# Kernel tuning notes

Measured on AMD Instinct MI355X. Metric: run time of the kernel, lower is better.

Reference implementation:

```python
import jax, jax.numpy as jnp
import numpy as np

BN_EPS = 1e-5

def conv2d(x, w, pad):
    return jax.lax.conv_general_dilated(x, w, (1, 1), [(pad, pad), (pad, pad)],
                                        dimension_numbers=('NCHW', 'OIHW', 'NCHW'))

def bn(x, g, b, m, v):
    # eval-mode batchnorm with running stats
    c = (None, slice(None), None, None)
    return g[c] * (x - m[c]) * jax.lax.rsqrt(v[c] + BN_EPS) + b[c]

def criss_cross_attention(x, wq, wk, wv, gamma):
    # x: (B, C, H, W); q/k have reduced dim d = C//8
    B, C, H, W = x.shape
    q = jnp.einsum('bchw,dc->bdhw', x, wq)
    k = jnp.einsum('bchw,dc->bdhw', x, wk)
    v = jnp.einsum('bchw,dc->bdhw', x, wv)
    # column (vertical) affinities: for each (h,w), keys at (k,w) -> (B,H,W,H)
    eH = jnp.einsum('bdhw,bdkw->bhwk', q, k)
    # -inf on the h==k diagonal (avoid counting the center pixel twice)
    eH = eH + jnp.where(jnp.eye(H, dtype=bool), -jnp.inf, 0.0)[None, :, None, :]
    # row (horizontal) affinities: keys at (h,k) -> (B,H,W,W)
    eW = jnp.einsum('bdhw,bdhk->bhwk', q, k)
    att = jax.nn.softmax(jnp.concatenate([eH, eW], axis=3), axis=3)  # (B,H,W,H+W)
    aH, aW = att[..., :H], att[..., H:]
    oH = jnp.einsum('bhwk,bdkw->bdhw', aH, v)
    oW = jnp.einsum('bhwk,bdhk->bdhw', aW, v)
    return gamma * (oH + oW) + x

def upsample_bilinear_align_corners(x, out_h, out_w):
    # torch nn.Upsample(mode='bilinear', align_corners=True)
    def interp(x, size, axis):
        n = x.shape[axis]
        pos = jnp.arange(size, dtype=x.dtype) * ((n - 1) / (size - 1))
        lo = jnp.floor(pos).astype(jnp.int32)
        hi = jnp.minimum(lo + 1, n - 1)
        w = pos - lo.astype(x.dtype)
        shp = [1] * x.ndim; shp[axis] = size
        w = w.reshape(shp)
        return jnp.take(x, lo, axis=axis) * (1 - w) + jnp.take(x, hi, axis=axis) * w
    x = interp(x, out_h, 2)
    return interp(x, out_w, 3)

def setup_inputs() -> dict:
    key = jax.random.key(0)
    ks = jax.random.split(key, 16)
    B, C, H, W = 2, 2048, 96, 96
    ic = C // 32          # inter_c = 64
    dq = ic // 8          # 8
    nc = 19
    s = 0.05
    return {
        'x': jax.random.normal(ks[0], (B, C, H, W), jnp.float32),
        'w_in': jax.random.normal(ks[1], (ic, C, 3, 3), jnp.float32) * s,
        'bn_in_g': jnp.ones((ic,), jnp.float32),
        'bn_in_b': jnp.zeros((ic,), jnp.float32),
        'bn_in_m': jax.random.normal(ks[2], (ic,), jnp.float32) * 0.1,
        'bn_in_v': jax.random.uniform(ks[3], (ic,), jnp.float32, 0.5, 1.5),
        'wq': jax.random.normal(ks[4], (dq, ic), jnp.float32) * s,
        'wk': jax.random.normal(ks[5], (dq, ic), jnp.float32) * s,
        'wv': jax.random.normal(ks[6], (ic, ic), jnp.float32) * s,
        'cca_gamma': jax.random.uniform(ks[7], (1,), jnp.float32, 0.2, 0.8),
        'w_out': jax.random.normal(ks[8], (ic, ic, 3, 3), jnp.float32) * s,
        'bn_out_g': jnp.ones((ic,), jnp.float32),
        'bn_out_b': jnp.zeros((ic,), jnp.float32),
        'bn_out_m': jax.random.normal(ks[9], (ic,), jnp.float32) * 0.1,
        'bn_out_v': jax.random.uniform(ks[10], (ic,), jnp.float32, 0.5, 1.5),
        'w_cls1': jax.random.normal(ks[11], (ic, C + ic, 3, 3), jnp.float32) * s,
        'bn_cls_g': jnp.ones((ic,), jnp.float32),
        'bn_cls_b': jnp.zeros((ic,), jnp.float32),
        'bn_cls_m': jax.random.normal(ks[12], (ic,), jnp.float32) * 0.1,
        'bn_cls_v': jax.random.uniform(ks[13], (ic,), jnp.float32, 0.5, 1.5),
        'w_cls2': jax.random.normal(ks[14], (nc, ic, 1, 1), jnp.float32) * s,
    }

def reference(x, w_in, bn_in_g, bn_in_b, bn_in_m, bn_in_v,
              wq, wk, wv, cca_gamma,
              w_out, bn_out_g, bn_out_b, bn_out_m, bn_out_v,
              w_cls1, bn_cls_g, bn_cls_b, bn_cls_m, bn_cls_v, w_cls2):
    RECURRENCE = 2
    out = jax.nn.relu(bn(conv2d(x, w_in, 1), bn_in_g, bn_in_b, bn_in_m, bn_in_v))
    for _ in range(RECURRENCE):
        out = criss_cross_attention(out, wq, wk, wv, cca_gamma)
    out = jax.nn.relu(bn(conv2d(out, w_out, 1), bn_out_g, bn_out_b, bn_out_m, bn_out_v))
    out = jnp.concatenate([x, out], axis=1)
    # cls_seg: conv -> BN (no relu) -> upsample x8 (bilinear, align_corners) -> 1x1 conv
    out = bn(conv2d(out, w_cls1, 1), bn_cls_g, bn_cls_b, bn_cls_m, bn_cls_v)
    H, W = out.shape[2], out.shape[3]
    out = upsample_bilinear_align_corners(out, H * 8, W * 8)
    out = conv2d(out, w_cls2, 0)
    return out
```

## Files before the change

### kernel.cpp

```cpp
#include <hip/hip_runtime.h>
#include <stdint.h>

#define HW 9216

typedef float f32x4 __attribute__((ext_vector_type(4)));
typedef short s16x8 __attribute__((ext_vector_type(8)));

#define PIN() asm volatile("" ::: "memory")
#define WAITV12() asm volatile("s_waitcnt vmcnt(12)" ::: "memory")

__device__ __forceinline__ unsigned short f2bf(float f){
  union { float fv; uint32_t u; } x; x.fv = f;
  uint32_t u = x.u;
  u += 0x7fffu + ((u >> 16) & 1u);
  return (unsigned short)(u >> 16);
}
__device__ __forceinline__ float bf2f(unsigned short s){
  union { uint32_t u; float fv; } x; x.u = ((uint32_t)s) << 16;
  return x.fv;
}

__device__ __forceinline__ void gload16(const void* g, void* l){
  __builtin_amdgcn_global_load_lds(
    (const __attribute__((address_space(1))) unsigned int*)g,
    (__attribute__((address_space(3))) unsigned int*)l, 16, 0, 0);
}

__global__ __launch_bounds__(256) void transp_kernel(const float* __restrict__ x,
    unsigned short* __restrict__ xT){
  __shared__ unsigned short tl[256 * 66];
  int blk = blockIdx.x;
  int b = blk / 1152; int r = blk - b * 1152;
  int cchunk = r / 144, pxt = r - cchunk * 144;
  int c0 = cchunk * 256, px0 = pxt * 64;
  int tid = threadIdx.x;
  for (int e = tid; e < 4096; e += 256){
    int cc = e >> 4, pq = e & 15;
    float4 v4 = *(const float4*)(x + ((size_t)(b * 2048 + c0 + cc)) * HW + px0 + pq * 4);
    const float* vp = (const float*)&v4;
    #pragma unroll
    for (int j = 0; j < 4; j++) tl[cc * 66 + pq * 4 + j] = f2bf(vp[j]);
  }
  __syncthreads();
  for (int j = tid; j < 2048; j += 256){
    int px = j >> 5, oct = j & 31;
    s16x8 pk;
    #pragma unroll
    for (int t = 0; t < 8; t++) pk[t] = (short)tl[(oct * 8 + t) * 66 + px];
    *(s16x8*)(xT + ((size_t)(b * 9216 + px0 + px)) * 2048 + c0 + oct * 8) = pk;
  }
}

__global__ void packw_kernel(const float* __restrict__ w, unsigned short* __restrict__ Wp, int Cin){
  int total = 64 * Cin * 9;
  for (int i = blockIdx.x * blockDim.x + threadIdx.x; i < total; i += gridDim.x * blockDim.x){
    int c = i & 31; int r = i >> 5; int o = r & 63; int r2 = r >> 6;
    int tap = r2 % 9; int ck = r2 / 9;
    Wp[i] = f2bf(w[((size_t)o * Cin + ck * 32 + c) * 9 + tap]);
  }
}

template<int T>
__device__ __forceinline__ void tapbody(const char* hb, s16x8 (&bs)[4], f32x4 (&acc)[4][4],
    const unsigned short* wbase, int gmax, int g0, int wv, int ln, int kg){
  constexpr int dy = T / 3, dx = T - dy * 3;
  #pragma unroll
  for (int mf = 0; mf < 4; mf++){
    int p = (wv * 4 + mf + dy) * 18 + (ln + dx);
    int aoff = p * 64 + ((kg ^ (p & 3)) << 4);
    s16x8 a = *(const s16x8*)(hb + aoff);
    #pragma unroll
    for (int nf = 0; nf < 4; nf++)
      acc[mf][nf] = __builtin_amdgcn_mfma_f32_16x16x32_bf16(a, bs[nf], acc[mf][nf], 0, 0, 0);
  }
  constexpr int dck = (T + 3) / 9, dt = (T + 3) % 9;
  if (g0 + T + 3 < gmax){
    const unsigned short* wb2 = wbase + dck * 18432 + dt * 2048;
    #pragma unroll
    for (int nf = 0; nf < 4; nf++) bs[nf] = *(const s16x8*)(wb2 + nf * 512);
  }
}

__global__ __launch_bounds__(256, 2) void conv_nhwc_kernel(
    const unsigned short* __restrict__ A0, int c0stride,
    const unsigned short* __restrict__ A1, int nck0,
    const unsigned short* __restrict__ Wp,
    unsigned short* __restrict__ sl, int nchunks,
    const unsigned short* __restrict__ zp){
  int mt = blockIdx.x;
  int b = mt / 36; int r = mt - b * 36;
  int h0 = (r / 6) * 16, w0 = (r % 6) * 16;
  int KS = gridDim.y, ks = blockIdx.y;
  int c0 = (nchunks * ks) / KS, c1 = (nchunks * (ks + 1)) / KS;
  int tid = threadIdx.x, lane = tid & 63, wv = tid >> 6;
  int ln = lane & 15, kg = lane >> 4;
  __shared__ char halo[2][24576];

  int pixb0[6], pixb1[6]; bool val[6];
  #pragma unroll
  for (int rr = 0; rr < 6; rr++){
    int i = tid + rr * 256;
    int p = i >> 2, q_lds = i & 3;
    int logq = q_lds ^ (p & 3);
    int hh = p / 18, ww = p - hh * 18;
    int h = h0 - 1 + hh, w = w0 - 1 + ww;
    bool v = (i < 1296) && ((unsigned)h < 96u) && ((unsigned)w < 96u);
    val[rr] = v;
    int pix = (b * 96 + h) * 96 + w;
    pixb0[rr] = v ? (pix * c0stride * 2 + logq * 16) : 0;
    pixb1[rr] = v ? (pix * 128 + logq * 16) : 0;
  }
  const char* a0B = (const char*)A0;
  const char* a1B = (const char*)A1;
  const char* zpB = (const char*)zp;

  auto stage = [&](char* ldsB, int ck){
    bool inA0 = (ck < nck0);
    int chb0 = ck * 64, chb1 = (ck - nck0) * 64;
    #pragma unroll
    for (int rr = 0; rr < 6; rr++){
      const char* src = zpB;
      if (val[rr]) src = inA0 ? (a0B + pixb0[rr] + chb0) : (a1B + pixb1[rr] + chb1);
      gload16(src, ldsB + (tid + rr * 256) * 16);
    }
  };

  f32x4 acc[4][4];
  #pragma unroll
  for (int i = 0; i < 4; i++)
    #pragma unroll
    for (int j = 0; j < 4; j++) acc[i][j] = (f32x4)(0.f);

  s16x8 bs0[4], bs1[4], bs2[4];
  int gmax = (c1 - c0) * 9;

  stage(&halo[0][0], c0);
  PIN();
  {
    const unsigned short* w0b = Wp + (size_t)c0 * 18432 + ln * 32 + kg * 8;
    #pragma unroll
    for (int nf = 0; nf < 4; nf++){
      bs0[nf] = *(const s16x8*)(w0b + 0 * 2048 + nf * 512);
      bs1[nf] = *(const s16x8*)(w0b + 1 * 2048 + nf * 512);
      bs2[nf] = *(const s16x8*)(w0b + 2 * 2048 + nf * 512);
    }
  }
  WAITV12();
  __builtin_amdgcn_s_barrier();

  for (int ck = c0; ck < c1; ck++){
    int cur = (ck - c0) & 1;
    if (ck + 1 < c1){ stage(&halo[cur ^ 1][0], ck + 1); PIN(); }
    const unsigned short* wbase = Wp + (size_t)ck * 18432 + ln * 32 + kg * 8;
    const char* hb = &halo[cur][0];
    int g0 = (ck - c0) * 9;
    tapbody<0>(hb, bs0, acc, wbase, gmax, g0, wv, ln, kg);
    tapbody<1>(hb, bs1, acc, wbase, gmax, g0, wv, ln, kg);
    tapbody<2>(hb, bs2, acc, wbase, gmax, g0, wv, ln, kg);
    tapbody<3>(hb, bs0, acc, wbase, gmax, g0, wv, ln, kg);
    tapbody<4>(hb, bs1, acc, wbase, gmax, g0, wv, ln, kg);
    tapbody<5>(hb, bs2, acc, wbase, gmax, g0, wv, ln, kg);
    tapbody<6>(hb, bs0, acc, wbase, gmax, g0, wv, ln, kg);
    tapbody<7>(hb, bs1, acc, wbase, gmax, g0, wv, ln, kg);
    tapbody<8>(hb, bs2, acc, wbase, gmax, g0, wv, ln, kg);
    if (ck + 1 < c1){
      WAITV12();
      __builtin_amdgcn_s_barrier();
    }
  }

  unsigned short* base = sl + ((size_t)(ks * 72 + mt)) * 16384;
  #pragma unroll
  for (int mf = 0; mf < 4; mf++)
    #pragma unroll
    for (int nf = 0; nf < 4; nf++){
      int o = nf * 16 + ln;
      #pragma unroll
      for (int rr = 0; rr < 4; rr++){
        int m = wv * 64 + mf * 16 + kg * 4 + rr;
        base[m * 64 + o] = f2bf(acc[mf][nf][rr]);
      }
    }
}

__global__ __launch_bounds__(256) void bn_reduce_kernel(const unsigned short* __restrict__ sl,
    int KS, const float* __restrict__ g, const float* __restrict__ bb,
    const float* __restrict__ mm, const float* __restrict__ vv, int relu,
    unsigned short* __restrict__ out){
  int idx = blockIdx.x * 256 + threadIdx.x;
  int mt = idx >> 14, e = idx & 16383;
  int m = e >> 6, o = e & 63;
  float s = 0.f;
  for (int ks = 0; ks < KS; ks++) s += bf2f(sl[((size_t)(ks * 72 + mt)) * 16384 + e]);
  float sc = g[o] * rsqrtf(vv[o] + 1e-5f);
  float valf = (s - mm[o]) * sc + bb[o];
  if (relu) valf = fmaxf(valf, 0.f);
  int b = mt / 36; int r = mt - b * 36;
  int h = (r / 6) * 16 + (m >> 4), w = (r % 6) * 16 + (m & 15);
  out[(((size_t)b * 96 + h) * 96 + w) * 64 + o] = f2bf(valf);
}

__global__ __launch_bounds__(256) void bn_reduce_cls_kernel(const unsigned short* __restrict__ sl,
    int KS, const float* __restrict__ g, const float* __restrict__ bb,
    const float* __restrict__ mm, const float* __restrict__ vv,
    const float* __restrict__ w2, float* __restrict__ t19){
  __shared__ float yl[4][64];
  __shared__ float w2L[19 * 64];
  int tid = threadIdx.x;
  for (int i = tid; i < 1216; i += 256) w2L[i] = w2[i];
  int idx = blockIdx.x * 256 + tid;
  int mt = idx >> 14, e = idx & 16383;
  int o = e & 63;
  float s = 0.f;
  for (int ks = 0; ks < KS; ks++) s += bf2f(sl[((size_t)(ks * 72 + mt)) * 16384 + e]);
  float sc = g[o] * rsqrtf(vv[o] + 1e-5f);
  float valf = (s - mm[o]) * sc + bb[o];
  yl[tid >> 6][o] = valf;
  __syncthreads();
  if (tid < 76){
    int mq = tid / 19, j = tid - mq * 19;
    float a = 0.f;
    #pragma unroll 8
    for (int c = 0; c < 64; c++) a += w2L[j * 64 + c] * yl[mq][c];
    int m = ((blockIdx.x & 63) << 2) + mq;
    int b = mt / 36; int r = mt - b * 36;
    int h = (r / 6) * 16 + (m >> 4), w = (r % 6) * 16 + (m & 15);
    t19[((size_t)(b * 19 + j)) * HW + h * 96 + w] = a;
  }
}

__global__ __launch_bounds__(128) void cca_proj_kernel(const unsigned short* __restrict__ xin,
    const float* __restrict__ wq, const float* __restrict__ wk, const float* __restrict__ wv,
    float* __restrict__ q, float* __restrict__ k, float* __restrict__ v){
  __shared__ float wqL[512], wkL[512], wvL[4096];
  int tid = threadIdx.x;
  for (int i = tid; i < 512; i += 128){ wqL[i] = wq[i]; wkL[i] = wk[i]; }
  for (int i = tid; i < 4096; i += 128) wvL[i] = wv[i];
  __syncthreads();
  int gp = blockIdx.x * 128 + tid;
  unsigned short xv16[64];
  #pragma unroll
  for (int t = 0; t < 8; t++)
    *(s16x8*)(&xv16[t * 8]) = *(const s16x8*)(xin + (size_t)gp * 64 + t * 8);
  float qa[8], ka[8], va[64];
  #pragma unroll
  for (int d = 0; d < 8; d++){ qa[d] = 0.f; ka[d] = 0.f; }
  #pragma unroll
  for (int d = 0; d < 64; d++) va[d] = 0.f;
  #pragma unroll 4
  for (int c = 0; c < 64; c++){
    float xv = bf2f(xv16[c]);
    #pragma unroll
    for (int d = 0; d < 8; d++){ qa[d] += wqL[d * 64 + c] * xv; ka[d] += wkL[d * 64 + c] * xv; }
    #pragma unroll
    for (int d = 0; d < 64; d++) va[d] += wvL[d * 64 + c] * xv;
  }
  #pragma unroll
  for (int d = 0; d < 8; d++){ q[(size_t)gp * 8 + d] = qa[d]; k[(size_t)gp * 8 + d] = ka[d]; }
  #pragma unroll
  for (int d = 0; d < 64; d++) v[(size_t)gp * 64 + d] = va[d];
}

__global__ __launch_bounds__(256, 2) void cca_colE_kernel(const float* __restrict__ qT,
    const float* __restrict__ kT, float* __restrict__ ebuf){
  int blk = blockIdx.x; int b = blk / 96, w = blk - b * 96;
  __shared__ float qcL[96 * 12], kcL[96 * 12];
  int tid = threadIdx.x;
  for (int i = tid; i < 768; i += 256){
    int hp = i >> 3, d = i & 7;
    size_t gidx = ((size_t)(b * HW) + hp * 96 + w) * 8 + d;
    qcL[hp * 12 + d] = qT[gidx];
    kcL[hp * 12 + d] = kT[gidx];
  }
  __syncthreads();
  int hb = tid & 15, kb2 = tid >> 4;
  int h0 = hb * 6, kp0 = kb2 * 6;
  f32x4 q0[6], q1[6], k0[6], k1[6];
  #pragma unroll
  for (int i = 0; i < 6; i++){
    q0[i] = *(const f32x4*)&qcL[(h0 + i) * 12];
    q1[i] = *(const f32x4*)&qcL[(h0 + i) * 12 + 4];
    k0[i] = *(const f32x4*)&kcL[(kp0 + i) * 12];
    k1[i] = *(const f32x4*)&kcL[(kp0 + i) * 12 + 4];
  }
  #pragma unroll
  for (int i = 0; i < 6; i++){
    size_t rbase = (((size_t)b * 96 + (h0 + i)) * 96 + w) * 96;
    #pragma unroll
    for (int j = 0; j < 6; j++){
      float e = 0.f;
      #pragma unroll
      for (int d = 0; d < 4; d++) e += q0[i][d] * k0[j][d] + q1[i][d] * k1[j][d];
      ebuf[rbase + kp0 + j] = (kp0 + j == h0 + i) ? -1e30f : e;
    }
  }
}

__global__ __launch_bounds__(256, 1) void cca_rowSM_kernel(const float* __restrict__ qT,
    const float* __restrict__ kT, const float* __restrict__ vT,
    const unsigned short* __restrict__ xin, const float* __restrict__ gamma,
    float* __restrict__ ebuf, unsigned short* __restrict__ xout){
  int blk = blockIdx.x; int b = blk / 96, h = blk - b * 96;
  __shared__ float qrL[96 * 12], krL[96 * 12];
  __shared__ float ewT[96 * 102];
  __shared__ unsigned short vL2[96 * 68];
  __shared__ unsigned short aW[96 * 100];
  int tid = threadIdx.x;
  int lane = tid & 63, wvid = tid >> 6;
  size_t rowb = (size_t)(b * HW) + h * 96;
  const float* ebase = ebuf + rowb * 96;

  float pre0[24], pre1[24];
  #pragma unroll
  for (int t = 0; t < 24; t++){
    int w = wvid + t * 4;
    pre0[t] = ebase[(size_t)w * 96 + lane];
    pre1[t] = (lane < 32) ? ebase[(size_t)w * 96 + 64 + lane] : 0.f;
  }

  for (int i = tid; i < 768; i += 256){
    int wp = i >> 3, d = i & 7;
    qrL[wp * 12 + d] = qT[(rowb + wp) * 8 + d];
    krL[wp * 12 + d] = kT[(rowb + wp) * 8 + d];
  }
  for (int i = tid; i < 6144; i += 256){
    int wp = i >> 6, d = i & 63;
    vL2[wp * 68 + d] = f2bf(vT[(rowb + wp) * 64 + d]);
  }
  __syncthreads();
  {
    int wb_ = tid & 15, kb_ = tid >> 4;
    int w0 = wb_ * 6, kp0 = kb_ * 6;
    f32x4 q0[6], q1[6], k0[6], k1[6];
    #pragma unroll
    for (int i = 0; i < 6; i++){
      q0[i] = *(const f32x4*)&qrL[(w0 + i) * 12];
      q1[i] = *(const f32x4*)&qrL[(w0 + i) * 12 + 4];
      k0[i] = *(const f32x4*)&krL[(kp0 + i) * 12];
      k1[i] = *(const f32x4*)&krL[(kp0 + i) * 12 + 4];
    }
    #pragma unroll
    for (int j = 0; j < 6; j++)
      #pragma unroll
      for (int i = 0; i < 6; i++){
        float e = 0.f;
        #pragma unroll
        for (int d = 0; d < 4; d++) e += q0[i][d] * k0[j][d] + q1[i][d] * k1[j][d];
        ewT[(kp0 + j) * 102 + (w0 + i)] = e;
      }
  }
  __syncthreads();
  #pragma unroll
  for (int t = 0; t < 24; t++){
    int w = wvid + t * 4;
    float x0 = pre0[t];
    float x1 = (lane < 32) ? pre1[t] : ewT[(lane - 32) * 102 + w];
    float x2 = ewT[(lane + 32) * 102 + w];
    float mx = fmaxf(x0, fmaxf(x1, x2));
    #pragma unroll
    for (int s = 32; s; s >>= 1) mx = fmaxf(mx, __shfl_xor(mx, s));
    float e0 = __expf(x0 - mx), e1 = __expf(x1 - mx), e2 = __expf(x2 - mx);
    float sm = e0 + e1 + e2;
    #pragma unroll
    for (int s = 32; s; s >>= 1) sm += __shfl_xor(sm, s);
    float inv = 1.f / sm;
    float* ebw = (float*)(ebase + (size_t)w * 96);
    ebw[lane] = e0 * inv;
    if (lane < 32) ebw[64 + lane] = e1 * inv;
    else           aW[(lane - 32) * 100 + w] = f2bf(e1 * inv);
    aW[(lane + 32) * 100 + w] = f2bf(e2 * inv);
  }
  __syncthreads();
  float gm = gamma[0];
  int d0 = (tid & 15) * 4, w0 = (tid >> 4) * 6;
  f32x4 acc2[6];
  #pragma unroll
  for (int c = 0; c < 6; c++) acc2[c] = (f32x4)(0.f);
  for (int kp = 0; kp < 96; kp++){
    ushort4 vv4 = *(const ushort4*)&vL2[kp * 68 + d0];
    f32x4 vf; vf[0] = bf2f(vv4.x); vf[1] = bf2f(vv4.y); vf[2] = bf2f(vv4.z); vf[3] = bf2f(vv4.w);
    ushort2 a01 = *(const ushort2*)&aW[kp * 100 + w0];
    ushort2 a23 = *(const ushort2*)&aW[kp * 100 + w0 + 2];
    ushort2 a45 = *(const ushort2*)&aW[kp * 100 + w0 + 4];
    acc2[0] += vf * bf2f(a01.x); acc2[1] += vf * bf2f(a01.y);
    acc2[2] += vf * bf2f(a23.x); acc2[3] += vf * bf2f(a23.y);
    acc2[4] += vf * bf2f(a45.x); acc2[5] += vf * bf2f(a45.y);
  }
  #pragma unroll
  for (int c = 0; c < 6; c++){
    size_t pix = rowb + (w0 + c);
    ushort4 xr = *(const ushort4*)&xin[pix * 64 + d0];
    ushort4 ov;
    ov.x = f2bf(bf2f(xr.x) + gm * acc2[c][0]);
    ov.y = f2bf(bf2f(xr.y) + gm * acc2[c][1]);
    ov.z = f2bf(bf2f(xr.z) + gm * acc2[c][2]);
    ov.w = f2bf(bf2f(xr.w) + gm * acc2[c][3]);
    *(ushort4*)&xout[pix * 64 + d0] = ov;
  }
}

__global__ __launch_bounds__(256, 2) void cca_colO_kernel(const float* __restrict__ vT,
    const float* __restrict__ gamma, const float* __restrict__ ebuf,
    const unsigned short* __restrict__ xpart, unsigned short* __restrict__ xout){
  int blk = blockIdx.x; int b = blk / 96, w = blk - b * 96;
  __shared__ unsigned short vL2[96 * 68];
  __shared__ unsigned short aTb[96 * 100];
  int tid = threadIdx.x;
  for (int i = tid; i < 6144; i += 256){
    int kp = i >> 6, d = i & 63;
    vL2[kp * 68 + d] = f2bf(vT[((size_t)(b * HW) + kp * 96 + w) * 64 + d]);
  }
  for (int i = tid; i < 9216; i += 256){
    int hh = i / 96, kp = i - hh * 96;
    aTb[kp * 100 + hh] = f2bf(ebuf[(((size_t)b * 96 + hh) * 96 + w) * 96 + kp]);
  }
  __syncthreads();
  float gm = gamma[0];
  int d0 = (tid & 15) * 4, h0 = (tid >> 4) * 6;
  f32x4 acc2[6];
  #pragma unroll
  for (int c = 0; c < 6; c++) acc2[c] = (f32x4)(0.f);
  for (int kp = 0; kp < 96; kp++){
    ushort4 vv4 = *(const ushort4*)&vL2[kp * 68 + d0];
    f32x4 vf; vf[0] = bf2f(vv4.x); vf[1] = bf2f(vv4.y); vf[2] = bf2f(vv4.z); vf[3] = bf2f(vv4.w);
    ushort2 a01 = *(const ushort2*)&aTb[kp * 100 + h0];
    ushort2 a23 = *(const ushort2*)&aTb[kp * 100 + h0 + 2];
    ushort2 a45 = *(const ushort2*)&aTb[kp * 100 + h0 + 4];
    acc2[0] += vf * bf2f(a01.x); acc2[1] += vf * bf2f(a01.y);
    acc2[2] += vf * bf2f(a23.x); acc2[3] += vf * bf2f(a23.y);
    acc2[4] += vf * bf2f(a45.x); acc2[5] += vf * bf2f(a45.y);
  }
  #pragma unroll
  for (int c = 0; c < 6; c++){
    size_t pix = (size_t)(b * HW) + (h0 + c) * 96 + w;
    ushort4 xr = *(const ushort4*)&xpart[pix * 64 + d0];
    ushort4 ov;
    ov.x = f2bf(bf2f(xr.x) + gm * acc2[c][0]);
    ov.y = f2bf(bf2f(xr.y) + gm * acc2[c][1]);
    ov.z = f2bf(bf2f(xr.z) + gm * acc2[c][2]);
    ov.w = f2bf(bf2f(xr.w) + gm * acc2[c][3]);
    *(ushort4*)&xout[pix * 64 + d0] = ov;
  }
}

__global__ void upsample_kernel(const float* __restrict__ t19, float* __restrict__ out){
  int gid = blockIdx.x * 256 + threadIdx.x;
  int xq = gid % 192; int t = gid / 192;
  int yy = t % 768; t /= 768;
  int o = t % 19; int b = t / 19;
  const float R = 95.0f / 767.0f;
  float ry = yy * R;
  int iy = (int)ry;
  float fy = ry - (float)iy;
  int iy1 = min(iy + 1, 95);
  const float* base = t19 + ((size_t)b * 19 + o) * HW;
  float4 res;
  float* rp = (float*)&res;
  #pragma unroll
  for (int j = 0; j < 4; j++){
    int xx = xq * 4 + j;
    float rx = xx * R;
    int ix = (int)rx; float fx = rx - (float)ix; int ix1 = min(ix + 1, 95);
    float v00 = base[iy * 96 + ix],  v01 = base[iy * 96 + ix1];
    float v10 = base[iy1 * 96 + ix], v11 = base[iy1 * 96 + ix1];
    rp[j] = (1.f - fy) * ((1.f - fx) * v00 + fx * v01) + fy * ((1.f - fx) * v10 + fx * v11);
  }
  *(float4*)(out + (((size_t)b * 19 + o) * 768 + yy) * 768 + xq * 4) = res;
}

extern "C" void kernel_launch(void* const* d_in, const int* in_sizes, int n_in,
                              void* d_out, int out_size, void* d_ws, size_t ws_size,
                              hipStream_t stream){
  const float* x       = (const float*)d_in[0];
  const float* w_in    = (const float*)d_in[1];
  const float* bn_in_g = (const float*)d_in[2];
  const float* bn_in_b = (const float*)d_in[3];
  const float* bn_in_m = (const float*)d_in[4];
  const float* bn_in_v = (const float*)d_in[5];
  const float* wq      = (const float*)d_in[6];
  const float* wk      = (const float*)d_in[7];
  const float* wv      = (const float*)d_in[8];
  const float* gamma   = (const float*)d_in[9];
  const float* w_out   = (const float*)d_in[10];
  const float* bn_o_g  = (const float*)d_in[11];
  const float* bn_o_b  = (const float*)d_in[12];
  const float* bn_o_m  = (const float*)d_in[13];
  const float* bn_o_v  = (const float*)d_in[14];
  const float* w_cls1  = (const float*)d_in[15];
  const float* bn_c_g  = (const float*)d_in[16];
  const float* bn_c_b  = (const float*)d_in[17];
  const float* bn_c_m  = (const float*)d_in[18];
  const float* bn_c_v  = (const float*)d_in[19];
  const float* w_cls2  = (const float*)d_in[20];
  float* out = (float*)d_out;

  char* ws = (char*)d_ws;
  size_t off = 0;
  auto alloc = [&](size_t bytes) -> void* {
    void* p = ws + off; off += (bytes + 255) & ~(size_t)255; return p;
  };
  const int KS = 12;
  const size_t NHWCb = (size_t)2 * HW * 64 * 2;
  unsigned short* xT   = (unsigned short*)alloc((size_t)2 * HW * 2048 * 2);
  unsigned short* sl   = (unsigned short*)alloc((size_t)KS * 72 * 16384 * 2);
  float* ebuf = (float*)sl;
  unsigned short* xattA = (unsigned short*)alloc(NHWCb);
  unsigned short* xattB = (unsigned short*)alloc(NHWCb);
  unsigned short* Ptmp  = (unsigned short*)alloc(NHWCb);
  unsigned short* attT  = (unsigned short*)alloc(NHWCb);
  unsigned short* midT  = (unsigned short*)alloc(NHWCb);
  float* qb    = (float*)alloc((size_t)2 * HW * 8 * 4);
  float* kb    = (float*)alloc((size_t)2 * HW * 8 * 4);
  float* vb    = (float*)alloc((size_t)2 * HW * 64 * 4);
  float* t19   = (float*)alloc((size_t)2 * 19 * HW * 4);
  unsigned short* WpIn  = (unsigned short*)alloc((size_t)64 * 2048 * 9 * 2);
  unsigned short* WpOut = (unsigned short*)alloc((size_t)64 * 64 * 9 * 2);
  unsigned short* WpCls = (unsigned short*)alloc((size_t)64 * 2112 * 9 * 2);
  unsigned short* zp    = (unsigned short*)alloc(256);
  (void)ws_size; (void)in_sizes; (void)n_in; (void)out_size;

  hipMemsetAsync(zp, 0, 256, stream);
  transp_kernel<<<2304, 256, 0, stream>>>(x, xT);
  packw_kernel<<<1024, 256, 0, stream>>>(w_in,   WpIn,  2048);
  packw_kernel<<<64,   256, 0, stream>>>(w_out,  WpOut, 64);
  packw_kernel<<<1024, 256, 0, stream>>>(w_cls1, WpCls, 2112);

  conv_nhwc_kernel<<<dim3(72, KS), 256, 0, stream>>>(xT, 2048, nullptr, 64, WpIn, sl, 64, zp);
  bn_reduce_kernel<<<4608, 256, 0, stream>>>(sl, KS, bn_in_g, bn_in_b, bn_in_m, bn_in_v, 1, xattA);

  cca_proj_kernel<<<144, 128, 0, stream>>>(xattA, wq, wk, wv, qb, kb, vb);
  cca_colE_kernel<<<192, 256, 0, stream>>>(qb, kb, ebuf);
  cca_rowSM_kernel<<<192, 256, 0, stream>>>(qb, kb, vb, xattA, gamma, ebuf, Ptmp);
  cca_colO_kernel<<<192, 256, 0, stream>>>(vb, gamma, ebuf, Ptmp, xattB);
  cca_proj_kernel<<<144, 128, 0, stream>>>(xattB, wq, wk, wv, qb, kb, vb);
  cca_colE_kernel<<<192, 256, 0, stream>>>(qb, kb, ebuf);
  cca_rowSM_kernel<<<192, 256, 0, stream>>>(qb, kb, vb, xattB, gamma, ebuf, Ptmp);
  cca_colO_kernel<<<192, 256, 0, stream>>>(vb, gamma, ebuf, Ptmp, attT);

  conv_nhwc_kernel<<<dim3(72, 2), 256, 0, stream>>>(attT, 64, nullptr, 2, WpOut, sl, 2, zp);
  bn_reduce_kernel<<<4608, 256, 0, stream>>>(sl, 2, bn_o_g, bn_o_b, bn_o_m, bn_o_v, 1, midT);

  conv_nhwc_kernel<<<dim3(72, KS), 256, 0, stream>>>(xT, 2048, midT, 64, WpCls, sl, 66, zp);
  bn_reduce_cls_kernel<<<4608, 256, 0, stream>>>(sl, KS, bn_c_g, bn_c_b, bn_c_m, bn_c_v, w_cls2, t19);

  upsample_kernel<<<21888, 256, 0, stream>>>(t19, out);
}
```

Measured before the change: 480.7 us.

## Fuse the input conv and cls conv into one 128-output-channel conv pass

The two 3x3 convolutions that both read the 2048-channel input are merged into one kernel. It packs both weight sets into a 128-output-channel layout, so each staged input halo feeds 8 MFMA column fragments instead of 4. The cls conv's extra 64 mid-channels become a separate small conv whose partials are summed in the cls BN reduction. The criss-cross attention kernels are also split into half-row/half-column blocks (384 blocks instead of 192), and the projection kernel is split across two threads per pixel, to raise parallelism. The cost is higher register pressure from the 4x8 accumulator tile and a larger split-K scratch buffer.

```diff
diff --git a/kernel.cpp b/kernel.cpp
--- a/kernel.cpp
+++ b/kernel.cpp
@@ -8,6 +8,7 @@
 
 #define PIN() asm volatile("" ::: "memory")
 #define WAITV12() asm volatile("s_waitcnt vmcnt(12)" ::: "memory")
+#define WAITV16() asm volatile("s_waitcnt vmcnt(16)" ::: "memory")
 
 __device__ __forceinline__ unsigned short f2bf(float f){
   union { float fv; uint32_t u; } x; x.fv = f;
@@ -51,6 +52,18 @@
   }
 }
 
+__global__ void pack2_kernel(const float* __restrict__ w_in, const float* __restrict__ w_cls1,
+    unsigned short* __restrict__ W2){
+  int total = 64 * 9 * 128 * 32;
+  for (int i = blockIdx.x * blockDim.x + threadIdx.x; i < total; i += gridDim.x * blockDim.x){
+    int c = i & 31; int o = (i >> 5) & 127; int r2 = i >> 12;
+    int tap = r2 % 9; int ck = r2 / 9;
+    int cin = ck * 32 + c;
+    float v = (o < 64) ? w_in[((size_t)o * 2048 + cin) * 9 + tap]
+                       : w_cls1[((size_t)(o - 64) * 2112 + cin) * 9 + tap];
+    W2[i] = f2bf(v);
+  }
+}
 __global__ void packw_kernel(const float* __restrict__ w, unsigned short* __restrict__ Wp, int Cin){
   int total = 64 * Cin * 9;
   for (int i = blockIdx.x * blockDim.x + threadIdx.x; i < total; i += gridDim.x * blockDim.x){
@@ -59,6 +72,135 @@
     Wp[i] = f2bf(w[((size_t)o * Cin + ck * 32 + c) * 9 + tap]);
   }
 }
+__global__ void packmid_kernel(const float* __restrict__ w_cls1, unsigned short* __restrict__ Wp){
+  int total = 2 * 9 * 64 * 32;
+  for (int i = blockIdx.x * blockDim.x + threadIdx.x; i < total; i += gridDim.x * blockDim.x){
+    int c = i & 31; int o = (i >> 5) & 63; int r2 = i >> 11;
+    int tap = r2 % 9; int ck2 = r2 / 9;
+    int cin = 2048 + ck2 * 32 + c;
+    Wp[i] = f2bf(w_cls1[((size_t)o * 2112 + cin) * 9 + tap]);
+  }
+}
+
+template<int T>
+__device__ __forceinline__ void tapstep(const char* hb, s16x8 (&slot)[8], f32x4 (&acc)[4][8],
+    const unsigned short* wbase, int gmax, int g0, int wv, int ln, int kg){
+  constexpr int dy = T / 3, dx = T - dy * 3;
+  #pragma unroll
+  for (int mf = 0; mf < 4; mf++){
+    int p = (wv * 4 + mf + dy) * 18 + (ln + dx);
+    int aoff = p * 64 + ((kg ^ (p & 3)) << 4);
+    s16x8 a = *(const s16x8*)(hb + aoff);
+    #pragma unroll
+    for (int nf = 0; nf < 8; nf++)
+      acc[mf][nf] = __builtin_amdgcn_mfma_f32_16x16x32_bf16(a, slot[nf], acc[mf][nf], 0, 0, 0);
+  }
+  constexpr int dck = (T + 2) / 9, dt = (T + 2) % 9;
+  if (g0 + T + 2 < gmax){
+    const unsigned short* wb2 = wbase + dck * 36864 + dt * 4096;
+    #pragma unroll
+    for (int nf = 0; nf < 8; nf++) slot[nf] = *(const s16x8*)(wb2 + nf * 512);
+  }
+}
+
+__global__ __launch_bounds__(256, 2) void conv_fused_kernel(
+    const unsigned short* __restrict__ A0,
+    const unsigned short* __restrict__ W2,
+    unsigned short* __restrict__ sl2,
+    const unsigned short* __restrict__ zp){
+  int mt = blockIdx.x;
+  int b = mt / 36; int r = mt - b * 36;
+  int h0 = (r / 6) * 16, w0 = (r % 6) * 16;
+  int KS = gridDim.y, ks = blockIdx.y;
+  int c0 = (64 * ks) / KS, c1 = (64 * (ks + 1)) / KS;
+  int tid = threadIdx.x, lane = tid & 63, wv = tid >> 6;
+  int ln = lane & 15, kg = lane >> 4;
+  __shared__ char halo[2][24576];
+
+  int pixb0[6]; bool val[6];
+  #pragma unroll
+  for (int rr = 0; rr < 6; rr++){
+    int i = tid + rr * 256;
+    int p = i >> 2, q_lds = i & 3;
+    int logq = q_lds ^ (p & 3);
+    int hh = p / 18, ww = p - hh * 18;
+    int h = h0 - 1 + hh, w = w0 - 1 + ww;
+    bool v = (i < 1296) && ((unsigned)h < 96u) && ((unsigned)w < 96u);
+    val[rr] = v;
+    int pix = (b * 96 + h) * 96 + w;
+    pixb0[rr] = v ? (pix * 4096 + logq * 16) : 0;
+  }
+  const char* a0B = (const char*)A0;
+  const char* zpB = (const char*)zp;
+
+  auto stage = [&](char* ldsB, int ck){
+    int chb0 = ck * 64;
+    #pragma unroll
+    for (int rr = 0; rr < 6; rr++){
+      const char* src = val[rr] ? (a0B + pixb0[rr] + chb0) : zpB;
+      gload16(src, ldsB + (tid + rr * 256) * 16);
+    }
+  };
+
+  f32x4 acc[4][8];
+  #pragma unroll
+  for (int i = 0; i < 4; i++)
+    #pragma unroll
+    for (int j = 0; j < 8; j++) acc[i][j] = (f32x4)(0.f);
+
+  s16x8 bsA[8], bsB[8];
+  int gmax = (c1 - c0) * 9;
+
+  stage(&halo[0][0], c0);
+  PIN();
+  {
+    const unsigned short* w0b = W2 + (size_t)c0 * 36864 + ln * 32 + kg * 8;
+    #pragma unroll
+    for (int nf = 0; nf < 8; nf++){
+      bsA[nf] = *(const s16x8*)(w0b + nf * 512);
+      bsB[nf] = *(const s16x8*)(w0b + 4096 + nf * 512);
+    }
+  }
+  WAITV16();
+  __builtin_amdgcn_s_barrier();
+
+  auto chunkbody = [&](int ck, s16x8 (&sE)[8], s16x8 (&sO)[8]){
+    const unsigned short* wbase = W2 + (size_t)ck * 36864 + ln * 32 + kg * 8;
+    const char* hb = &halo[(ck - c0) & 1][0];
+    int g0 = (ck - c0) * 9;
+    tapstep<0>(hb, sE, acc, wbase, gmax, g0, wv, ln, kg);
+    tapstep<1>(hb, sO, acc, wbase, gmax, g0, wv, ln, kg);
+    tapstep<2>(hb, sE, acc, wbase, gmax, g0, wv, ln, kg);
+    tapstep<3>(hb, sO, acc, wbase, gmax, g0, wv, ln, kg);
+    tapstep<4>(hb, sE, acc, wbase, gmax, g0, wv, ln, kg);
+    tapstep<5>(hb, sO, acc, wbase, gmax, g0, wv, ln, kg);
+    tapstep<6>(hb, sE, acc, wbase, gmax, g0, wv, ln, kg);
+    tapstep<7>(hb, sO, acc, wbase, gmax, g0, wv, ln, kg);
+    tapstep<8>(hb, sE, acc, wbase, gmax, g0, wv, ln, kg);
+  };
+
+  for (int ck = c0; ck < c1; ck++){
+    if (ck + 1 < c1){ stage(&halo[(ck - c0 + 1) & 1][0], ck + 1); PIN(); }
+    if ((ck - c0) & 1) chunkbody(ck, bsB, bsA); else chunkbody(ck, bsA, bsB);
+    if (ck + 1 < c1){
+      WAITV16();
+      __builtin_amdgcn_s_barrier();
+    }
+  }
+
+  unsigned short* base = sl2 + ((size_t)(ks * 72 + mt)) * 32768;
+  #pragma unroll
+  for (int mf = 0; mf < 4; mf++)
+    #pragma unroll
+    for (int nf = 0; nf < 8; nf++){
+      int o = nf * 16 + ln;
+      #pragma unroll
+      for (int rr = 0; rr < 4; rr++){
+        int m = wv * 64 + mf * 16 + kg * 4 + rr;
+        base[m * 128 + o] = f2bf(acc[mf][nf][rr]);
+      }
+    }
+}
 
 template<int T>
 __device__ __forceinline__ void tapbody(const char* hb, s16x8 (&bs)[4], f32x4 (&acc)[4][4],
@@ -83,7 +225,6 @@
 
 __global__ __launch_bounds__(256, 2) void conv_nhwc_kernel(
     const unsigned short* __restrict__ A0, int c0stride,
-    const unsigned short* __restrict__ A1, int nck0,
     const unsigned short* __restrict__ Wp,
     unsigned short* __restrict__ sl, int nchunks,
     const unsigned short* __restrict__ zp){
@@ -96,7 +237,7 @@
   int ln = lane & 15, kg = lane >> 4;
   __shared__ char halo[2][24576];
 
-  int pixb0[6], pixb1[6]; bool val[6];
+  int pixb0[6]; bool val[6];
   #pragma unroll
   for (int rr = 0; rr < 6; rr++){
     int i = tid + rr * 256;
@@ -108,19 +249,15 @@
     val[rr] = v;
     int pix = (b * 96 + h) * 96 + w;
     pixb0[rr] = v ? (pix * c0stride * 2 + logq * 16) : 0;
-    pixb1[rr] = v ? (pix * 128 + logq * 16) : 0;
   }
   const char* a0B = (const char*)A0;
-  const char* a1B = (const char*)A1;
   const char* zpB = (const char*)zp;
 
   auto stage = [&](char* ldsB, int ck){
-    bool inA0 = (ck < nck0);
-    int chb0 = ck * 64, chb1 = (ck - nck0) * 64;
+    int chb0 = ck * 64;
     #pragma unroll
     for (int rr = 0; rr < 6; rr++){
-      const char* src = zpB;
-      if (val[rr]) src = inA0 ? (a0B + pixb0[rr] + chb0) : (a1B + pixb1[rr] + chb1);
+      const char* src = val[rr] ? (a0B + pixb0[rr] + chb0) : zpB;
       gload16(src, ldsB + (tid + rr * 256) * 16);
     }
   };
@@ -183,6 +320,23 @@
     }
 }
 
+__global__ __launch_bounds__(256) void bn_reduce128_kernel(const unsigned short* __restrict__ sl2,
+    int KS, const float* __restrict__ g, const float* __restrict__ bb,
+    const float* __restrict__ mm, const float* __restrict__ vv, int relu,
+    unsigned short* __restrict__ out){
+  int idx = blockIdx.x * 256 + threadIdx.x;
+  int mt = idx >> 14, e = idx & 16383;
+  int m = e >> 6, o = e & 63;
+  float s = 0.f;
+  for (int ks = 0; ks < KS; ks++) s += bf2f(sl2[((size_t)(ks * 72 + mt) * 256 + m) * 128 + o]);
+  float sc = g[o] * rsqrtf(vv[o] + 1e-5f);
+  float valf = (s - mm[o]) * sc + bb[o];
+  if (relu) valf = fmaxf(valf, 0.f);
+  int b = mt / 36; int r = mt - b * 36;
+  int h = (r / 6) * 16 + (m >> 4), w = (r % 6) * 16 + (m & 15);
+  out[(((size_t)b * 96 + h) * 96 + w) * 64 + o] = f2bf(valf);
+}
+
 __global__ __launch_bounds__(256) void bn_reduce_kernel(const unsigned short* __restrict__ sl,
     int KS, const float* __restrict__ g, const float* __restrict__ bb,
     const float* __restrict__ mm, const float* __restrict__ vv, int relu,
@@ -200,8 +354,9 @@
   out[(((size_t)b * 96 + h) * 96 + w) * 64 + o] = f2bf(valf);
 }
 
-__global__ __launch_bounds__(256) void bn_reduce_cls_kernel(const unsigned short* __restrict__ sl,
-    int KS, const float* __restrict__ g, const float* __restrict__ bb,
+__global__ __launch_bounds__(256) void bn_reduce_cls_kernel(const unsigned short* __restrict__ sl2,
+    int KS, const unsigned short* __restrict__ midsl,
+    const float* __restrict__ g, const float* __restrict__ bb,
     const float* __restrict__ mm, const float* __restrict__ vv,
     const float* __restrict__ w2, float* __restrict__ t19){
   __shared__ float yl[4][64];
@@ -210,9 +365,10 @@
   for (int i = tid; i < 1216; i += 256) w2L[i] = w2[i];
   int idx = blockIdx.x * 256 + tid;
   int mt = idx >> 14, e = idx & 16383;
-  int o = e & 63;
+  int m = e >> 6, o = e & 63;
   float s = 0.f;
-  for (int ks = 0; ks < KS; ks++) s += bf2f(sl[((size_t)(ks * 72 + mt)) * 16384 + e]);
+  for (int ks = 0; ks < KS; ks++) s += bf2f(sl2[((size_t)(ks * 72 + mt) * 256 + m) * 128 + 64 + o]);
+  for (int k2 = 0; k2 < 2; k2++) s += bf2f(midsl[((size_t)(k2 * 72 + mt)) * 16384 + e]);
   float sc = g[o] * rsqrtf(vv[o] + 1e-5f);
   float valf = (s - mm[o]) * sc + bb[o];
   yl[tid >> 6][o] = valf;
@@ -222,105 +378,117 @@
     float a = 0.f;
     #pragma unroll 8
     for (int c = 0; c < 64; c++) a += w2L[j * 64 + c] * yl[mq][c];
-    int m = ((blockIdx.x & 63) << 2) + mq;
+    int mm2 = ((blockIdx.x & 63) << 2) + mq;
     int b = mt / 36; int r = mt - b * 36;
-    int h = (r / 6) * 16 + (m >> 4), w = (r % 6) * 16 + (m & 15);
+    int h = (r / 6) * 16 + (mm2 >> 4), w = (r % 6) * 16 + (mm2 & 15);
     t19[((size_t)(b * 19 + j)) * HW + h * 96 + w] = a;
   }
 }
 
-__global__ __launch_bounds__(128) void cca_proj_kernel(const unsigned short* __restrict__ xin,
+__global__ __launch_bounds__(256) void cca_proj_kernel(const unsigned short* __restrict__ xin,
     const float* __restrict__ wq, const float* __restrict__ wk, const float* __restrict__ wv,
     float* __restrict__ q, float* __restrict__ k, float* __restrict__ v){
   __shared__ float wqL[512], wkL[512], wvL[4096];
   int tid = threadIdx.x;
-  for (int i = tid; i < 512; i += 128){ wqL[i] = wq[i]; wkL[i] = wk[i]; }
-  for (int i = tid; i < 4096; i += 128) wvL[i] = wv[i];
+  for (int i = tid; i < 512; i += 256){ wqL[i] = wq[i]; wkL[i] = wk[i]; }
+  for (int i = tid; i < 4096; i += 256) wvL[i] = wv[i];
   __syncthreads();
-  int gp = blockIdx.x * 128 + tid;
+  int gid = blockIdx.x * 256 + tid;
+  int gp = gid >> 1, half = gid & 1;
   unsigned short xv16[64];
   #pragma unroll
   for (int t = 0; t < 8; t++)
     *(s16x8*)(&xv16[t * 8]) = *(const s16x8*)(xin + (size_t)gp * 64 + t * 8);
-  float qa[8], ka[8], va[64];
-  #pragma unroll
-  for (int d = 0; d < 8; d++){ qa[d] = 0.f; ka[d] = 0.f; }
-  #pragma unroll
-  for (int d = 0; d < 64; d++) va[d] = 0.f;
+  float qa[4], ka[4], va[32];
+  #pragma unroll
+  for (int d = 0; d < 4; d++){ qa[d] = 0.f; ka[d] = 0.f; }
+  #pragma unroll
+  for (int d = 0; d < 32; d++) va[d] = 0.f;
+  int qo = half * 4, vo = half * 32;
   #pragma unroll 4
   for (int c = 0; c < 64; c++){
     float xv = bf2f(xv16[c]);
     #pragma unroll
-    for (int d = 0; d < 8; d++){ qa[d] += wqL[d * 64 + c] * xv; ka[d] += wkL[d * 64 + c] * xv; }
-    #pragma unroll
-    for (int d = 0; d < 64; d++) va[d] += wvL[d * 64 + c] * xv;
-  }
-  #pragma unroll
-  for (int d = 0; d < 8; d++){ q[(size_t)gp * 8 + d] = qa[d]; k[(size_t)gp * 8 + d] = ka[d]; }
-  #pragma unroll
-  for (int d = 0; d < 64; d++) v[(size_t)gp * 64 + d] = va[d];
+    for (int d = 0; d < 4; d++){ qa[d] += wqL[(qo + d) * 64 + c] * xv; ka[d] += wkL[(qo + d) * 64 + c] * xv; }
+    #pragma unroll
+    for (int d = 0; d < 32; d++) va[d] += wvL[(vo + d) * 64 + c] * xv;
+  }
+  #pragma unroll
+  for (int d = 0; d < 4; d++){ q[(size_t)gp * 8 + qo + d] = qa[d]; k[(size_t)gp * 8 + qo + d] = ka[d]; }
+  #pragma unroll
+  for (int d = 0; d < 32; d++) v[(size_t)gp * 64 + vo + d] = va[d];
 }
 
 __global__ __launch_bounds__(256, 2) void cca_colE_kernel(const float* __restrict__ qT,
     const float* __restrict__ kT, float* __restrict__ ebuf){
-  int blk = blockIdx.x; int b = blk / 96, w = blk - b * 96;
-  __shared__ float qcL[96 * 12], kcL[96 * 12];
+  int blk = blockIdx.x;
+  int b = blk / 192; int r = blk - b * 192; int w = r >> 1, z = r & 1;
+  __shared__ float qcL[96 * 12], kcL[48 * 12];
   int tid = threadIdx.x;
   for (int i = tid; i < 768; i += 256){
     int hp = i >> 3, d = i & 7;
-    size_t gidx = ((size_t)(b * HW) + hp * 96 + w) * 8 + d;
-    qcL[hp * 12 + d] = qT[gidx];
-    kcL[hp * 12 + d] = kT[gidx];
+    qcL[hp * 12 + d] = qT[((size_t)(b * HW) + hp * 96 + w) * 8 + d];
+  }
+  for (int i = tid; i < 384; i += 256){
+    int j = i >> 3, d = i & 7;
+    kcL[j * 12 + d] = kT[((size_t)(b * HW) + (z * 48 + j) * 96 + w) * 8 + d];
   }
   __syncthreads();
-  int hb = tid & 15, kb2 = tid >> 4;
-  int h0 = hb * 6, kp0 = kb2 * 6;
-  f32x4 q0[6], q1[6], k0[6], k1[6];
+  int h0 = (tid & 15) * 6, kl0 = (tid >> 4) * 3;
+  f32x4 q0[6], q1[6], k0[3], k1[3];
   #pragma unroll
   for (int i = 0; i < 6; i++){
     q0[i] = *(const f32x4*)&qcL[(h0 + i) * 12];
     q1[i] = *(const f32x4*)&qcL[(h0 + i) * 12 + 4];
-    k0[i] = *(const f32x4*)&kcL[(kp0 + i) * 12];
-    k1[i] = *(const f32x4*)&kcL[(kp0 + i) * 12 + 4];
+  }
+  #pragma unroll
+  for (int j = 0; j < 3; j++){
+    k0[j] = *(const f32x4*)&kcL[(kl0 + j) * 12];
+    k1[j] = *(const f32x4*)&kcL[(kl0 + j) * 12 + 4];
   }
   #pragma unroll
   for (int i = 0; i < 6; i++){
     size_t rbase = (((size_t)b * 96 + (h0 + i)) * 96 + w) * 96;
     #pragma unroll
-    for (int j = 0; j < 6; j++){
+    for (int j = 0; j < 3; j++){
       float e = 0.f;
       #pragma unroll
       for (int d = 0; d < 4; d++) e += q0[i][d] * k0[j][d] + q1[i][d] * k1[j][d];
-      ebuf[rbase + kp0 + j] = (kp0 + j == h0 + i) ? -1e30f : e;
-    }
-  }
-}
-
-__global__ __launch_bounds__(256, 1) void cca_rowSM_kernel(const float* __restrict__ qT,
+      int kpg = z * 48 + kl0 + j;
+      ebuf[rbase + kpg] = (kpg == h0 + i) ? -1e30f : e;
+    }
+  }
+}
+
+__global__ __launch_bounds__(256, 2) void cca_rowSM_kernel(const float* __restrict__ qT,
     const float* __restrict__ kT, const float* __restrict__ vT,
     const unsigned short* __restrict__ xin, const float* __restrict__ gamma,
     float* __restrict__ ebuf, unsigned short* __restrict__ xout){
-  int blk = blockIdx.x; int b = blk / 96, h = blk - b * 96;
-  __shared__ float qrL[96 * 12], krL[96 * 12];
-  __shared__ float ewT[96 * 102];
+  int blk = blockIdx.x;
+  int b = blk / 192; int r = blk - b * 192; int h = r >> 1, z = r & 1;
+  __shared__ float qrL[48 * 12], krL[96 * 12];
+  __shared__ float ewT[96 * 50];
   __shared__ unsigned short vL2[96 * 68];
-  __shared__ unsigned short aW[96 * 100];
+  __shared__ unsigned short aW[96 * 50];
   int tid = threadIdx.x;
   int lane = tid & 63, wvid = tid >> 6;
   size_t rowb = (size_t)(b * HW) + h * 96;
   const float* ebase = ebuf + rowb * 96;
 
-  float pre0[24], pre1[24];
-  #pragma unroll
-  for (int t = 0; t < 24; t++){
-    int w = wvid + t * 4;
+  float pre0[12], pre1[12];
+  #pragma unroll
+  for (int t = 0; t < 12; t++){
+    int w = z * 48 + wvid + t * 4;
     pre0[t] = ebase[(size_t)w * 96 + lane];
     pre1[t] = (lane < 32) ? ebase[(size_t)w * 96 + 64 + lane] : 0.f;
   }
 
+  for (int i = tid; i < 384; i += 256){
+    int wl = i >> 3, d = i & 7;
+    qrL[wl * 12 + d] = qT[(rowb + z * 48 + wl) * 8 + d];
+  }
   for (int i = tid; i < 768; i += 256){
     int wp = i >> 3, d = i & 7;
-    qrL[wp * 12 + d] = qT[(rowb + wp) * 8 + d];
     krL[wp * 12 + d] = kT[(rowb + wp) * 8 + d];
   }
   for (int i = tid; i < 6144; i += 256){
@@ -329,33 +497,36 @@
   }
   __syncthreads();
   {
-    int wb_ = tid & 15, kb_ = tid >> 4;
-    int w0 = wb_ * 6, kp0 = kb_ * 6;
-    f32x4 q0[6], q1[6], k0[6], k1[6];
-    #pragma unroll
-    for (int i = 0; i < 6; i++){
-      q0[i] = *(const f32x4*)&qrL[(w0 + i) * 12];
-      q1[i] = *(const f32x4*)&qrL[(w0 + i) * 12 + 4];
-      k0[i] = *(const f32x4*)&krL[(kp0 + i) * 12];
-      k1[i] = *(const f32x4*)&krL[(kp0 + i) * 12 + 4];
+    int wl0 = (tid & 15) * 3, kp0 = (tid >> 4) * 6;
+    f32x4 q0[3], q1[3], k0[6], k1[6];
+    #pragma unroll
+    for (int i = 0; i < 3; i++){
+      q0[i] = *(const f32x4*)&qrL[(wl0 + i) * 12];
+      q1[i] = *(const f32x4*)&qrL[(wl0 + i) * 12 + 4];
+    }
+    #pragma unroll
+    for (int j = 0; j < 6; j++){
+      k0[j] = *(const f32x4*)&krL[(kp0 + j) * 12];
+      k1[j] = *(const f32x4*)&krL[(kp0 + j) * 12 + 4];
     }
     #pragma unroll
     for (int j = 0; j < 6; j++)
       #pragma unroll
-      for (int i = 0; i < 6; i++){
+      for (int i = 0; i < 3; i++){
         float e = 0.f;
         #pragma unroll
         for (int d = 0; d < 4; d++) e += q0[i][d] * k0[j][d] + q1[i][d] * k1[j][d];
-        ewT[(kp0 + j) * 102 + (w0 + i)] = e;
+        ewT[(kp0 + j) * 50 + (wl0 + i)] = e;
       }
   }
   __syncthreads();
   #pragma unroll
-  for (int t = 0; t < 24; t++){
-    int w = wvid + t * 4;
+  for (int t = 0; t < 12; t++){
+    int wl = wvid + t * 4;
+    int w = z * 48 + wl;
     float x0 = pre0[t];
-    float x1 = (lane < 32) ? pre1[t] : ewT[(lane - 32) * 102 + w];
-    float x2 = ewT[(lane + 32) * 102 + w];
+    float x1 = (lane < 32) ? pre1[t] : ewT[(lane - 32) * 50 + wl];
+    float x2 = ewT[(lane + 32) * 50 + wl];
     float mx = fmaxf(x0, fmaxf(x1, x2));
     #pragma unroll
     for (int s = 32; s; s >>= 1) mx = fmaxf(mx, __shfl_xor(mx, s));
@@ -367,28 +538,25 @@
     float* ebw = (float*)(ebase + (size_t)w * 96);
     ebw[lane] = e0 * inv;
     if (lane < 32) ebw[64 + lane] = e1 * inv;
-    else           aW[(lane - 32) * 100 + w] = f2bf(e1 * inv);
-    aW[(lane + 32) * 100 + w] = f2bf(e2 * inv);
+    else           aW[(lane - 32) * 50 + wl] = f2bf(e1 * inv);
+    aW[(lane + 32) * 50 + wl] = f2bf(e2 * inv);
   }
   __syncthreads();
   float gm = gamma[0];
-  int d0 = (tid & 15) * 4, w0 = (tid >> 4) * 6;
-  f32x4 acc2[6];
-  #pragma unroll
-  for (int c = 0; c < 6; c++) acc2[c] = (f32x4)(0.f);
+  int d0 = (tid & 15) * 4, wl0 = (tid >> 4) * 3;
+  f32x4 acc2[3];
+  #pragma unroll
+  for (int c = 0; c < 3; c++) acc2[c] = (f32x4)(0.f);
   for (int kp = 0; kp < 96; kp++){
     ushort4 vv4 = *(const ushort4*)&vL2[kp * 68 + d0];
     f32x4 vf; vf[0] = bf2f(vv4.x); vf[1] = bf2f(vv4.y); vf[2] = bf2f(vv4.z); vf[3] = bf2f(vv4.w);
-    ushort2 a01 = *(const ushort2*)&aW[kp * 100 + w0];
-    ushort2 a23 = *(const ushort2*)&aW[kp * 100 + w0 + 2];
-    ushort2 a45 = *(const ushort2*)&aW[kp * 100 + w0 + 4];
-    acc2[0] += vf * bf2f(a01.x); acc2[1] += vf * bf2f(a01.y);
-    acc2[2] += vf * bf2f(a23.x); acc2[3] += vf * bf2f(a23.y);
-    acc2[4] += vf * bf2f(a45.x); acc2[5] += vf * bf2f(a45.y);
-  }
-  #pragma unroll
-  for (int c = 0; c < 6; c++){
-    size_t pix = rowb + (w0 + c);
+    acc2[0] += vf * bf2f(aW[kp * 50 + wl0]);
+    acc2[1] += vf * bf2f(aW[kp * 50 + wl0 + 1]);
+    acc2[2] += vf * bf2f(aW[kp * 50 + wl0 + 2]);
+  }
+  #pragma unroll
+  for (int c = 0; c < 3; c++){
+    size_t pix = rowb + z * 48 + wl0 + c;
     ushort4 xr = *(const ushort4*)&xin[pix * 64 + d0];
     ushort4 ov;
     ov.x = f2bf(bf2f(xr.x) + gm * acc2[c][0]);
@@ -402,37 +570,35 @@
 __global__ __launch_bounds__(256, 2) void cca_colO_kernel(const float* __restrict__ vT,
     const float* __restrict__ gamma, const float* __restrict__ ebuf,
     const unsigned short* __restrict__ xpart, unsigned short* __restrict__ xout){
-  int blk = blockIdx.x; int b = blk / 96, w = blk - b * 96;
+  int blk = blockIdx.x;
+  int b = blk / 192; int r = blk - b * 192; int w = r >> 1, z = r & 1;
   __shared__ unsigned short vL2[96 * 68];
-  __shared__ unsigned short aTb[96 * 100];
+  __shared__ unsigned short aTb[96 * 50];
   int tid = threadIdx.x;
   for (int i = tid; i < 6144; i += 256){
     int kp = i >> 6, d = i & 63;
     vL2[kp * 68 + d] = f2bf(vT[((size_t)(b * HW) + kp * 96 + w) * 64 + d]);
   }
-  for (int i = tid; i < 9216; i += 256){
-    int hh = i / 96, kp = i - hh * 96;
-    aTb[kp * 100 + hh] = f2bf(ebuf[(((size_t)b * 96 + hh) * 96 + w) * 96 + kp]);
+  for (int i = tid; i < 4608; i += 256){
+    int hl = i / 96, kp = i - hl * 96;
+    aTb[kp * 50 + hl] = f2bf(ebuf[(((size_t)b * 96 + z * 48 + hl) * 96 + w) * 96 + kp]);
   }
   __syncthreads();
   float gm = gamma[0];
-  int d0 = (tid & 15) * 4, h0 = (tid >> 4) * 6;
-  f32x4 acc2[6];
-  #pragma unroll
-  for (int c = 0; c < 6; c++) acc2[c] = (f32x4)(0.f);
+  int d0 = (tid & 15) * 4, hl0 = (tid >> 4) * 3;
+  f32x4 acc2[3];
+  #pragma unroll
+  for (int c = 0; c < 3; c++) acc2[c] = (f32x4)(0.f);
   for (int kp = 0; kp < 96; kp++){
     ushort4 vv4 = *(const ushort4*)&vL2[kp * 68 + d0];
     f32x4 vf; vf[0] = bf2f(vv4.x); vf[1] = bf2f(vv4.y); vf[2] = bf2f(vv4.z); vf[3] = bf2f(vv4.w);
-    ushort2 a01 = *(const ushort2*)&aTb[kp * 100 + h0];
-    ushort2 a23 = *(const ushort2*)&aTb[kp * 100 + h0 + 2];
-    ushort2 a45 = *(const ushort2*)&aTb[kp * 100 + h0 + 4];
-    acc2[0] += vf * bf2f(a01.x); acc2[1] += vf * bf2f(a01.y);
-    acc2[2] += vf * bf2f(a23.x); acc2[3] += vf * bf2f(a23.y);
-    acc2[4] += vf * bf2f(a45.x); acc2[5] += vf * bf2f(a45.y);
-  }
-  #pragma unroll
-  for (int c = 0; c < 6; c++){
-    size_t pix = (size_t)(b * HW) + (h0 + c) * 96 + w;
+    acc2[0] += vf * bf2f(aTb[kp * 50 + hl0]);
+    acc2[1] += vf * bf2f(aTb[kp * 50 + hl0 + 1]);
+    acc2[2] += vf * bf2f(aTb[kp * 50 + hl0 + 2]);
+  }
+  #pragma unroll
+  for (int c = 0; c < 3; c++){
+    size_t pix = (size_t)(b * HW) + (z * 48 + hl0 + c) * 96 + w;
     ushort4 xr = *(const ushort4*)&xpart[pix * 64 + d0];
     ushort4 ov;
     ov.x = f2bf(bf2f(xr.x) + gm * acc2[c][0]);
@@ -501,9 +667,10 @@
   };
   const int KS = 12;
   const size_t NHWCb = (size_t)2 * HW * 64 * 2;
-  unsigned short* xT   = (unsigned short*)alloc((size_t)2 * HW * 2048 * 2);
-  unsigned short* sl   = (unsigned short*)alloc((size_t)KS * 72 * 16384 * 2);
-  float* ebuf = (float*)sl;
+  unsigned short* xT     = (unsigned short*)alloc((size_t)2 * HW * 2048 * 2);
+  unsigned short* sl2    = (unsigned short*)alloc((size_t)KS * 72 * 32768 * 2);
+  unsigned short* smallsl= (unsigned short*)alloc((size_t)2 * 72 * 16384 * 2);
+  float* ebuf  = (float*)alloc((size_t)2 * 96 * HW * 4);
   unsigned short* xattA = (unsigned short*)alloc(NHWCb);
   unsigned short* xattB = (unsigned short*)alloc(NHWCb);
   unsigned short* Ptmp  = (unsigned short*)alloc(NHWCb);
@@ -513,35 +680,37 @@
   float* kb    = (float*)alloc((size_t)2 * HW * 8 * 4);
   float* vb    = (float*)alloc((size_t)2 * HW * 64 * 4);
   float* t19   = (float*)alloc((size_t)2 * 19 * HW * 4);
-  unsigned short* WpIn  = (unsigned short*)alloc((size_t)64 * 2048 * 9 * 2);
+  unsigned short* W2    = (unsigned short*)alloc((size_t)64 * 9 * 128 * 32 * 2);
   unsigned short* WpOut = (unsigned short*)alloc((size_t)64 * 64 * 9 * 2);
-  unsigned short* WpCls = (unsigned short*)alloc((size_t)64 * 2112 * 9 * 2);
+  unsigned short* WpMid = (unsigned short*)alloc((size_t)2 * 9 * 64 * 32 * 2);
   unsigned short* zp    = (unsigned short*)alloc(256);
   (void)ws_size; (void)in_sizes; (void)n_in; (void)out_size;
 
   hipMemsetAsync(zp, 0, 256, stream);
   transp_kernel<<<2304, 256, 0, stream>>>(x, xT);
-  packw_kernel<<<1024, 256, 0, stream>>>(w_in,   WpIn,  2048);
-  packw_kernel<<<64,   256, 0, stream>>>(w_out,  WpOut, 64);
-  packw_kernel<<<1024, 256, 0, stream>>>(w_cls1, WpCls, 2112);
-
-  conv_nhwc_kernel<<<dim3(72, KS), 256, 0, stream>>>(xT, 2048, nullptr, 64, WpIn, sl, 64, zp);
-  bn_reduce_kernel<<<4608, 256, 0, stream>>>(sl, KS, bn_in_g, bn_in_b, bn_in_m, bn_in_v, 1, xattA);
-
-  cca_proj_kernel<<<144, 128, 0, stream>>>(xattA, wq, wk, wv, qb, kb, vb);
-  cca_colE_kernel<<<192, 256, 0, stream>>>(qb, kb, ebuf);
-  cca_rowSM_kernel<<<192, 256, 0, stream>>>(qb, kb, vb, xattA, gamma, ebuf, Ptmp);
-  cca_colO_kernel<<<192, 256, 0, stream>>>(vb, gamma, ebuf, Ptmp, xattB);
-  cca_proj_kernel<<<144, 128, 0, stream>>>(xattB, wq, wk, wv, qb, kb, vb);
-  cca_colE_kernel<<<192, 256, 0, stream>>>(qb, kb, ebuf);
-  cca_rowSM_kernel<<<192, 256, 0, stream>>>(qb, kb, vb, xattB, gamma, ebuf, Ptmp);
-  cca_colO_kernel<<<192, 256, 0, stream>>>(vb, gamma, ebuf, Ptmp, attT);
-
-  conv_nhwc_kernel<<<dim3(72, 2), 256, 0, stream>>>(attT, 64, nullptr, 2, WpOut, sl, 2, zp);
-  bn_reduce_kernel<<<4608, 256, 0, stream>>>(sl, 2, bn_o_g, bn_o_b, bn_o_m, bn_o_v, 1, midT);
-
-  conv_nhwc_kernel<<<dim3(72, KS), 256, 0, stream>>>(xT, 2048, midT, 64, WpCls, sl, 66, zp);
-  bn_reduce_cls_kernel<<<4608, 256, 0, stream>>>(sl, KS, bn_c_g, bn_c_b, bn_c_m, bn_c_v, w_cls2, t19);
+  pack2_kernel<<<1024, 256, 0, stream>>>(w_in, w_cls1, W2);
+  packw_kernel<<<64, 256, 0, stream>>>(w_out, WpOut, 64);
+  packmid_kernel<<<144, 256, 0, stream>>>(w_cls1, WpMid);
+
+  conv_fused_kernel<<<dim3(72, KS), 256, 0, stream>>>(xT, W2, sl2, zp);
+  bn_reduce128_kernel<<<4608, 256, 0, stream>>>(sl2, KS, bn_in_g, bn_in_b, bn_in_m, bn_in_v, 1, xattA);
+
+  cca_proj_kernel<<<144, 256, 0, stream>>>(xattA, wq, wk, wv, qb, kb, vb);
+  cca_colE_kernel<<<384, 256, 0, stream>>>(qb, kb, ebuf);
+  cca_rowSM_kernel<<<384, 256, 0, stream>>>(qb, kb, vb, xattA, gamma, ebuf, Ptmp);
+  cca_colO_kernel<<<384, 256, 0, stream>>>(vb, gamma, ebuf, Ptmp, xattB);
+  cca_proj_kernel<<<144, 256, 0, stream>>>(xattB, wq, wk, wv, qb, kb, vb);
+  cca_colE_kernel<<<384, 256, 0, stream>>>(qb, kb, ebuf);
+  cca_rowSM_kernel<<<384, 256, 0, stream>>>(qb, kb, vb, xattB, gamma, ebuf, Ptmp);
+  cca_colO_kernel<<<384, 256, 0, stream>>>(vb, gamma, ebuf, Ptmp, attT);
+
+  conv_nhwc_kernel<<<dim3(72, 2), 256, 0, stream>>>(attT, 64, WpOut, smallsl, 2, zp);
+  bn_reduce_kernel<<<4608, 256, 0, stream>>>(smallsl, 2, bn_o_g, bn_o_b, bn_o_m, bn_o_v, 1, midT);
+
+  conv_nhwc_kernel<<<dim3(72, 2), 256, 0, stream>>>(midT, 64, WpMid, smallsl, 2, zp);
+
+  bn_reduce_cls_kernel<<<4608, 256, 0, stream>>>(sl2, KS, smallsl,
+      bn_c_g, bn_c_b, bn_c_m, bn_c_v, w_cls2, t19);
 
   upsample_kernel<<<21888, 256, 0, stream>>>(t19, out);
 }
```

New measurement: 777.5 us. 61.7% more time.
